# Kernel optimization log

Measured on AMD Instinct MI355X. Metric: run time of the kernel, lower is better.

Reference implementation:

```python
import jax, jax.numpy as jnp
import numpy as np
import math

N = 20000          # nodes
E = 320000         # edges (avg degree 16)
NS, NV = 16, 4     # scalar / vector multiplicities
NCAT = 10
CAT_VOCAB = 119
DIST_DIM = 32
LIG_MAX_R = 5.0
W1_NUMEL = NS * NS + NS * NV          # 320 : layer1 tp weights
W2_NUMEL = NS * NS + NV * NS + NS * NV + NV * NV + NV * NV  # 416


def setup_inputs() -> dict:
    key = jax.random.key(0)
    ks = jax.random.split(key, 24)
    s = 0.1
    inp = {
        'x_cat': jax.random.randint(ks[0], (N, NCAT), 0, 2),
        'x_scalar': jax.random.normal(ks[1], (N, 32), jnp.float32),
        'pos': jax.random.normal(ks[2], (N, 3), jnp.float32) * 3.0,
        'edge_index': jax.random.randint(ks[3], (2, E), 0, N),
        'edge_bond': jax.random.uniform(ks[4], (E, 10), jnp.float32),
        # AtomEncoder params
        'emb_tables': jax.random.normal(ks[5], (NCAT, CAT_VOCAB, NS)) * s,
        'node_w': jax.random.normal(ks[6], (32, NS)) * s,
        'node_b': jnp.zeros((NS,), jnp.float32),
        # lig_edge_embedding MLP (42 -> ns -> ns)
        'em_w1': jax.random.normal(ks[7], (10 + DIST_DIM, NS)) * s,
        'em_b1': jnp.zeros((NS,), jnp.float32),
        'em_w2': jax.random.normal(ks[8], (NS, NS)) * s,
        'em_b2': jnp.zeros((NS,), jnp.float32),
        'c1_w1': jax.random.normal(ks[9], (3 * NS, 3 * NS)) * s,
        'c1_b1': jnp.zeros((3 * NS,), jnp.float32),
        'c1_w2': jax.random.normal(ks[10], (3 * NS, W1_NUMEL)) * s,
        'c1_b2': jnp.zeros((W1_NUMEL,), jnp.float32),
        # conv layer 2 fc
        'c2_w1': jax.random.normal(ks[11], (3 * NS, 3 * NS)) * s,
        'c2_b1': jnp.zeros((3 * NS,), jnp.float32),
        'c2_w2': jax.random.normal(ks[12], (3 * NS, W2_NUMEL)) * s,
        'c2_b2': jnp.zeros((W2_NUMEL,), jnp.float32),
    }
    return inp


def _scatter_mean(vals, idx, n):
    s = jax.ops.segment_sum(vals, idx, num_segments=n)
    cnt = jax.ops.segment_sum(jnp.ones(idx.shape, vals.dtype), idx, num_segments=n)
    return s / jnp.maximum(cnt, 1.0)[:, None]


def _forward(x_cat, x_scalar, pos, edge_index, edge_bond,
             emb_tables, node_w, node_b, em_w1, em_b1, em_w2, em_b2,
             c1_w1, c1_b1, c1_w2, c1_b2, c2_w1, c2_b1, c2_w2, c2_b2):
    ns, nv = NS, NV
    n = x_cat.shape[0]
    # ---- AtomEncoder: sum of categorical embeddings + linear(scalar) ----
    gathered = emb_tables[jnp.arange(NCAT)[None, :], x_cat]      # [N, 10, ns]
    node = gathered.sum(axis=1) + x_scalar @ node_w + node_b    # [N, ns]

    src, dst = edge_index[0], edge_index[1]
    vec = pos[dst] - pos[src]                                   # [E, 3]
    dist = jnp.sqrt(jnp.sum(vec * vec, axis=-1) + 1e-12)
    unit = vec / (dist + 1e-8)[:, None]
    # spherical harmonics, lmax=1, component normalization: [1, sqrt(3)*r_hat]
    sh0 = jnp.ones((vec.shape[0], 1), vec.dtype)
    sh1 = math.sqrt(3.0) * unit                                 # [E, 3]

    # ---- GaussianSmearing + edge embedding MLP ----
    offset = jnp.linspace(0.0, LIG_MAX_R, DIST_DIM)
    coeff = -0.5 / float(LIG_MAX_R / (DIST_DIM - 1)) ** 2
    demb = jnp.exp(coeff * (dist[:, None] - offset[None, :]) ** 2)
    e_in = jnp.concatenate([edge_bond, demb], axis=1)           # [E, 42]
    edge_emb = jax.nn.relu(e_in @ em_w1 + em_b1) @ em_w2 + em_b2  # [E, ns]

    # ======== conv layer 1: ns x0e -> ns x0e + nv x1o ========
    ea = jnp.concatenate([edge_emb, node[src, :ns], node[dst, :ns]], axis=1)
    w = jax.nn.relu(ea @ c1_w1 + c1_b1) @ c1_w2 + c1_b2         # [E, 320]
    wa = w[:, :ns * ns].reshape(-1, ns, ns)
    wb = w[:, ns * ns:].reshape(-1, ns, nv)
    s_dst = node[dst]                                           # [E, ns]
    a = 1.0 / math.sqrt(ns)                                     # fan-in norm
    out0 = jnp.einsum('euk,eu->ek', wa, s_dst) * sh0 * a        # 0e x 0e -> 0e
    out1 = jnp.einsum('euw,eu->ew', wb, s_dst)[:, :, None] * sh1[:, None, :] * a
    tp = jnp.concatenate([out0, out1.reshape(-1, 3 * nv)], axis=1)
    node = _scatter_mean(tp, src, n)                            # [N, ns+3nv]

    # ======== conv layer 2: ns x0e + nv x1o -> ns x0e + nv x1o + nv x1e ====
    ea = jnp.concatenate([edge_emb, node[src, :ns], node[dst, :ns]], axis=1)
    w = jax.nn.relu(ea @ c2_w1 + c2_b1) @ c2_w2 + c2_b2         # [E, 416]
    o = 0
    wa = w[:, o:o + ns * ns].reshape(-1, ns, ns); o += ns * ns
    wb = w[:, o:o + nv * ns].reshape(-1, nv, ns); o += nv * ns
    wc = w[:, o:o + ns * nv].reshape(-1, ns, nv); o += ns * nv
    wd = w[:, o:o + nv * nv].reshape(-1, nv, nv); o += nv * nv
    we = w[:, o:o + nv * nv].reshape(-1, nv, nv)
    s = node[dst, :ns]
    v = node[dst, ns:].reshape(-1, nv, 3)
    a0 = 1.0 / math.sqrt(ns + nv)   # two paths into 0e
    a1 = 1.0 / math.sqrt(ns + nv)   # two paths into 1o
    aE = 1.0 / math.sqrt(nv)        # one path into 1e
    vdot = jnp.einsum('evi,ei->ev', v, sh1)                     # 1o . 1o
    out0 = (jnp.einsum('euk,eu->ek', wa, s) * sh0
            + jnp.einsum('euk,eu->ek', wb, vdot) / math.sqrt(3.0)) * a0
    out1o = (jnp.einsum('euw,eu->ew', wc, s)[:, :, None] * sh1[:, None, :]
             + jnp.einsum('euw,eui->ewi', wd, v) * sh0[:, :, None]) * a1
    crossv = jnp.cross(v, jnp.broadcast_to(sh1[:, None, :], v.shape))
    out1e = jnp.einsum('euw,eui->ewi', we, crossv) * (aE / math.sqrt(2.0))
    tp = jnp.concatenate([out0, out1o.reshape(-1, 3 * nv),
                          out1e.reshape(-1, 3 * nv)], axis=1)
    node = _scatter_mean(tp, src, n)                            # [N, ns+6nv] = [N,40]
    return node


def reference(x_cat, x_scalar, pos, edge_index, edge_bond,
              emb_tables, node_w, node_b, em_w1, em_b1, em_w2, em_b2,
              c1_w1, c1_b1, c1_w2, c1_b2, c2_w1, c2_b1, c2_w2, c2_b2):
    return _forward(x_cat, x_scalar, pos, edge_index, edge_bond,
                    emb_tables, node_w, node_b, em_w1, em_b1, em_w2, em_b2,
                    c1_w1, c1_b1, c1_w2, c1_b2, c2_w1, c2_b1, c2_w2, c2_b2)
```

## Files before the change

kernel.cpp:

```cpp
#include <hip/hip_runtime.h>
#include <math.h>

#define NN 20000
#define NE 320000

typedef _Float16 f16x8 __attribute__((ext_vector_type(8)));
typedef float f32x4 __attribute__((ext_vector_type(4)));
typedef unsigned short ushort_t;
typedef unsigned int uint_t;

#define MFMA16(A,B,C) __builtin_amdgcn_mfma_f32_16x16x32_f16((A),(B),(C),0,0,0)
#define LDS_FENCE() do{ asm volatile("s_waitcnt lgkmcnt(0)" ::: "memory"); __builtin_amdgcn_sched_barrier(0);}while(0)

static_assert(NE % 64 == 0, "edge grid must tile exactly");

__device__ __forceinline__ float frelu(float x){ return fmaxf(x, 0.0f); }

__device__ __forceinline__ void splitf(float x, ushort_t& h, ushort_t& l){
    _Float16 hh = (_Float16)x;
    float r = (x - (float)hh) * 2048.0f;
    _Float16 ll = (_Float16)r;
    union { _Float16 f; ushort_t u; } ch, cl;
    ch.f = hh; cl.f = ll;
    h = ch.u; l = cl.u;
}

__device__ __forceinline__ void edge_embed(
    int e, int s, int d,
    const float* __restrict__ pos,
    const float* __restrict__ edge_bond,
    const float* __restrict__ em_w1, const float* __restrict__ em_b1,
    const float* __restrict__ em_w2, const float* __restrict__ em_b2,
    float* eemb, float* sh1)
{
    float vx = pos[d*3+0] - pos[s*3+0];
    float vy = pos[d*3+1] - pos[s*3+1];
    float vz = pos[d*3+2] - pos[s*3+2];
    float d2 = vx*vx + vy*vy + vz*vz + 1e-12f;
    float dist = sqrtf(d2);
    float inv = 1.0f / (dist + 1e-8f);
    const float SQ3 = 1.7320508075688772f;
    sh1[0] = SQ3 * vx * inv;
    sh1[1] = SQ3 * vy * inv;
    sh1[2] = SQ3 * vz * inv;

    float ein[42];
    #pragma unroll
    for (int t = 0; t < 10; ++t) ein[t] = edge_bond[e*10 + t];
    const float coeff = -19.22f;
    const float step  = 5.0f / 31.0f;
    #pragma unroll
    for (int k = 0; k < 32; ++k) {
        float dd = dist - step * (float)k;
        ein[10+k] = __expf(coeff * dd * dd);
    }

    float t1[16];
    #pragma unroll
    for (int j = 0; j < 16; ++j) t1[j] = em_b1[j];
    #pragma unroll
    for (int t = 0; t < 42; ++t) {
        float v = ein[t];
        #pragma unroll
        for (int j = 0; j < 16; ++j) t1[j] += v * em_w1[t*16 + j];
    }
    #pragma unroll
    for (int j = 0; j < 16; ++j) t1[j] = frelu(t1[j]);

    #pragma unroll
    for (int j = 0; j < 16; ++j) eemb[j] = em_b2[j];
    #pragma unroll
    for (int t = 0; t < 16; ++t) {
        float v = t1[t];
        #pragma unroll
        for (int j = 0; j < 16; ++j) eemb[j] += v * em_w2[t*16 + j];
    }
}

__global__ __launch_bounds__(256)
void k_node_y(const float* __restrict__ node, int stride,
              const float* __restrict__ w1, float* __restrict__ y)
{
    int n = blockIdx.x*256 + threadIdx.x;
    if (n >= NN) return;
    float sv[16];
    const float4* r = reinterpret_cast<const float4*>(node + (size_t)n*stride);
    #pragma unroll
    for (int k = 0; k < 4; ++k) {
        float4 q = r[k];
        sv[4*k]=q.x; sv[4*k+1]=q.y; sv[4*k+2]=q.z; sv[4*k+3]=q.w;
    }
    float yb[48];
    #pragma unroll
    for (int j = 0; j < 48; ++j) yb[j] = 0.f;
    #pragma unroll
    for (int t = 0; t < 16; ++t) {
        float v = sv[t];
        #pragma unroll
        for (int j = 0; j < 48; ++j) yb[j] += v * w1[(16+t)*48 + j];
    }
    float* yo = y + (size_t)n*96;
    #pragma unroll
    for (int j = 0; j < 12; ++j)
        reinterpret_cast<float4*>(yo)[j] = make_float4(yb[4*j], yb[4*j+1], yb[4*j+2], yb[4*j+3]);
    #pragma unroll
    for (int j = 0; j < 48; ++j) yb[j] = 0.f;
    #pragma unroll
    for (int t = 0; t < 16; ++t) {
        float v = sv[t];
        #pragma unroll
        for (int j = 0; j < 48; ++j) yb[j] += v * w1[(32+t)*48 + j];
    }
    #pragma unroll
    for (int j = 0; j < 12; ++j)
        reinterpret_cast<float4*>(yo + 48)[j] = make_float4(yb[4*j], yb[4*j+1], yb[4*j+2], yb[4*j+3]);
}

__global__ __launch_bounds__(256)
void k_pack(const float* __restrict__ w2, const float* __restrict__ b2,
            ushort_t* __restrict__ out, int NC, int ntiles)
{
    int slot = blockIdx.x*256 + threadIdx.x;
    if (slot >= ntiles*128) return;
    int tl = slot >> 7; int r7 = slot & 127; int kb = r7 >> 6; int ll = r7 & 63;
    int col = tl*16 + (ll & 15);
    int k0 = (kb<<5) + ((ll>>4)<<3);
    uint_t hw[4], lw[4];
    #pragma unroll
    for (int p = 0; p < 4; ++p) {
        int ka = k0 + 2*p, kb2 = k0 + 2*p + 1;
        float va = (ka < 48) ? w2[ka*NC + col] : (ka == 48 ? b2[col] : 0.0f);
        float vb = (kb2 < 48) ? w2[kb2*NC + col] : (kb2 == 48 ? b2[col] : 0.0f);
        ushort_t ah, al, bh, bl;
        splitf(va, ah, al);
        splitf(vb, bh, bl);
        hw[p] = (uint_t)ah | ((uint_t)bh << 16);
        lw[p] = (uint_t)al | ((uint_t)bl << 16);
    }
    int base = tl*2048 + kb*1024 + ll*8;
    *reinterpret_cast<uint4*>(&out[base])       = make_uint4(hw[0], hw[1], hw[2], hw[3]);
    *reinterpret_cast<uint4*>(&out[base + 512]) = make_uint4(lw[0], lw[1], lw[2], lw[3]);
}

struct B4 { f16x8 h0, l0, h1, l1; };
__device__ __forceinline__ B4 loadB(const f16x8* __restrict__ g, int t, int l) {
    B4 b;
    const f16x8* p = g + t*256 + l;
    b.h0 = p[0];
    b.l0 = p[64];
    b.h1 = p[128];
    b.l1 = p[192];
    return b;
}

__device__ __forceinline__ void stage_A(ushort_t* bounce, int l,
                                        const uint_t* hph, const uint_t* hpl,
                                        f16x8 ahi[4][2], f16x8 alo[4][2])
{
    #pragma unroll
    for (int t = 0; t < 4; ++t)
        *reinterpret_cast<uint4*>(&bounce[l*32 + t*8]) = make_uint4(0,0,0,0);
    LDS_FENCE();
    #pragma unroll
    for (int mt = 0; mt < 4; ++mt) {
        if ((l >> 4) == mt) {
            #pragma unroll
            for (int jj = 0; jj < 25; ++jj) {
                int k = jj*2, kb = k >> 5, kk = k & 31;
                int lr = (l & 15) + ((kk >> 3) << 4);
                int off = kb*512 + lr*8 + (kk & 7);
                *reinterpret_cast<uint_t*>(&bounce[off])        = hph[jj];
                *reinterpret_cast<uint_t*>(&bounce[1024 + off]) = hpl[jj];
            }
        }
        LDS_FENCE();
        ahi[mt][0] = *reinterpret_cast<const f16x8*>(&bounce[l*8]);
        ahi[mt][1] = *reinterpret_cast<const f16x8*>(&bounce[512 + l*8]);
        alo[mt][0] = *reinterpret_cast<const f16x8*>(&bounce[1024 + l*8]);
        alo[mt][1] = *reinterpret_cast<const f16x8*>(&bounce[1536 + l*8]);
        LDS_FENCE();
    }
}

__device__ __forceinline__ void build_h_reg(
    const float* em, int s, int d,
    const float* __restrict__ y,
    const float* __restrict__ w1, const float* __restrict__ b1,
    float* h)
{
    #pragma unroll
    for (int j = 0; j < 48; ++j) h[j] = b1[j];
    #pragma unroll
    for (int t = 0; t < 16; ++t) {
        float v = em[t];
        #pragma unroll
        for (int j = 0; j < 48; ++j) h[j] += v * w1[t*48 + j];
    }
    const float4* pb = reinterpret_cast<const float4*>(y + (size_t)s*96);
    const float4* pc = reinterpret_cast<const float4*>(y + (size_t)d*96 + 48);
    #pragma unroll
    for (int kk = 0; kk < 12; ++kk) {
        float4 qb = pb[kk], qc = pc[kk];
        h[4*kk+0] = frelu(h[4*kk+0] + qb.x + qc.x);
        h[4*kk+1] = frelu(h[4*kk+1] + qb.y + qc.y);
        h[4*kk+2] = frelu(h[4*kk+2] + qb.z + qc.z);
        h[4*kk+3] = frelu(h[4*kk+3] + qb.w + qc.w);
    }
}

__global__ __launch_bounds__(256)
void k_node_feat(const int* __restrict__ x_cat, const float* __restrict__ x_scalar,
                 const float* __restrict__ emb, const float* __restrict__ node_w,
                 const float* __restrict__ node_b, float* __restrict__ node0)
{
    int n = blockIdx.x * 256 + threadIdx.x;
    if (n >= NN) return;
    float acc[16];
    #pragma unroll
    for (int k = 0; k < 16; ++k) acc[k] = node_b[k];
    #pragma unroll
    for (int c = 0; c < 10; ++c) {
        int idx = x_cat[n*10 + c];
        const float4* row = reinterpret_cast<const float4*>(emb + (c*119 + idx)*16);
        #pragma unroll
        for (int k = 0; k < 4; ++k) {
            float4 q = row[k];
            acc[4*k+0] += q.x; acc[4*k+1] += q.y; acc[4*k+2] += q.z; acc[4*k+3] += q.w;
        }
    }
    #pragma unroll
    for (int t = 0; t < 32; ++t) {
        float xs = x_scalar[n*32 + t];
        #pragma unroll
        for (int k = 0; k < 16; ++k) acc[k] += xs * node_w[t*16 + k];
    }
    #pragma unroll
    for (int k = 0; k < 16; ++k) node0[n*16 + k] = acc[k];
}

__global__ __launch_bounds__(64)
void k_edge_l1(const int* __restrict__ ei, const float* __restrict__ pos,
               const float* __restrict__ edge_bond,
               const float* __restrict__ em_w1, const float* __restrict__ em_b1,
               const float* __restrict__ em_w2, const float* __restrict__ em_b2,
               const float* __restrict__ w1, const float* __restrict__ b1,
               const ushort_t* __restrict__ packW,
               const float* __restrict__ y,
               const float* __restrict__ node0,
               float* __restrict__ eembG, float* __restrict__ eshG,
               float* __restrict__ accum, float* __restrict__ cnt)
{
    __shared__ __align__(16) unsigned char smem[5376];
    float* sT  = (float*)smem;
    float* sSh = (float*)(smem + 4352);
    int*   sSrc= (int*)(smem + 5120);

    int l = threadIdx.x;
    int cc = l & 15;
    int e = blockIdx.x*64 + l;
    int s = ei[e], d = ei[NE + e];

    float em[16], sh1[3];
    edge_embed(e, s, d, pos, edge_bond, em_w1, em_b1, em_w2, em_b2, em, sh1);
    {
        float4* pe = reinterpret_cast<float4*>(eembG + (size_t)e*16);
        #pragma unroll
        for (int k = 0; k < 4; ++k)
            pe[k] = make_float4(em[4*k], em[4*k+1], em[4*k+2], em[4*k+3]);
        reinterpret_cast<float4*>(eshG)[e] = make_float4(sh1[0], sh1[1], sh1[2], 0.f);
    }
    atomicAdd(cnt + s, 1.0f);

    float sd[16];
    {
        const float4* rd = reinterpret_cast<const float4*>(node0 + (size_t)d*16);
        #pragma unroll
        for (int k = 0; k < 4; ++k) {
            float4 q = rd[k];
            sd[4*k]=q.x; sd[4*k+1]=q.y; sd[4*k+2]=q.z; sd[4*k+3]=q.w;
        }
    }
    float h[48];
    build_h_reg(em, s, d, y, w1, b1, h);

    uint_t hph[25], hpl[25];
    #pragma unroll
    for (int jj = 0; jj < 24; ++jj) {
        ushort_t ah, al, bh, bl;
        splitf(h[2*jj],   ah, al);
        splitf(h[2*jj+1], bh, bl);
        hph[jj] = (uint_t)ah | ((uint_t)bh << 16);
        hpl[jj] = (uint_t)al | ((uint_t)bl << 16);
    }
    hph[24] = 0x3C00u;
    hpl[24] = 0u;

    f16x8 ahi[4][2], alo[4][2];
    stage_A((ushort_t*)smem, l, hph, hpl, ahi, alo);

    LDS_FENCE();
    sSrc[l] = s;
    #pragma unroll
    for (int u = 0; u < 16; ++u) sT[u*68 + l] = sd[u];
    sSh[l*3+0] = sh1[0]; sSh[l*3+1] = sh1[1]; sSh[l*3+2] = sh1[2];
    LDS_FENCE();

    f32x4 out0[4];
    float ob[4][4];
    #pragma unroll
    for (int mt = 0; mt < 4; ++mt) {
        out0[mt] = (f32x4){0.f,0.f,0.f,0.f};
        #pragma unroll
        for (int r = 0; r < 4; ++r) ob[mt][r] = 0.f;
    }

    const f16x8* gB = reinterpret_cast<const f16x8*>(packW);

    auto process = [&](int t, const B4& cur) {
        #pragma unroll
        for (int mt = 0; mt < 4; ++mt) {
            f32x4 Dh = (f32x4){0.f,0.f,0.f,0.f};
            f32x4 Dc = (f32x4){0.f,0.f,0.f,0.f};
            Dh = MFMA16(ahi[mt][0], cur.h0, Dh);
            Dh = MFMA16(ahi[mt][1], cur.h1, Dh);
            Dc = MFMA16(alo[mt][0], cur.h0, Dc);
            Dc = MFMA16(ahi[mt][0], cur.l0, Dc);
            Dc = MFMA16(alo[mt][1], cur.h1, Dc);
            Dc = MFMA16(ahi[mt][1], cur.l1, Dc);
            f32x4 D = Dh + Dc * 0.00048828125f;
            int elb = (mt << 4) + ((l >> 4) << 2);
            if (t < 16) {
                f32x4 sv = *reinterpret_cast<const f32x4*>(&sT[t*68 + elb]);
                out0[mt] += sv * D;
            } else {
                const float* sp = &sT[(((t-16)<<2) + (cc>>2))*68 + elb];
                #pragma unroll
                for (int r = 0; r < 4; ++r) ob[mt][r] += sp[r] * D[r];
            }
        }
    };

    B4 b0 = loadB(gB, 0, l), b1v = loadB(gB, 1, l);
    #pragma unroll 1
    for (int t = 0; t < 20; t += 2) {
        B4 p0 = (t + 2 < 20) ? loadB(gB, t + 2, l) : b0;
        process(t, b0);
        B4 p1 = (t + 3 < 20) ? loadB(gB, t + 3, l) : b1v;
        process(t + 1, b1v);
        b0 = p0; b1v = p1;
    }

    #pragma unroll
    for (int mt = 0; mt < 4; ++mt) {
        int elb = (mt << 4) + ((l >> 4) << 2);
        #pragma unroll
        for (int r = 0; r < 4; ++r) {
            int el = elb + r;
            int sidx = sSrc[el];
            atomicAdd(accum + (size_t)sidx*28 + cc, out0[mt][r] * 0.25f);
            float x = ob[mt][r];
            x += __shfl_xor(x, 4); x += __shfl_xor(x, 8);
            int q = cc / 3; int i2 = cc - q*3;
            float xq = __shfl(x, (l & 48) | q);
            if (cc < 12)
                atomicAdd(accum + (size_t)sidx*28 + 16 + cc, 0.25f * xq * sSh[el*3 + i2]);
        }
    }
}

__global__ __launch_bounds__(64)
void k_edge_l2(const int* __restrict__ ei,
               const float* __restrict__ w1, const float* __restrict__ b1,
               const ushort_t* __restrict__ packW,
               const float* __restrict__ eembG, const float* __restrict__ eshG,
               const float* __restrict__ y,
               const float* __restrict__ node1,
               float* __restrict__ accum2)
{
    __shared__ __align__(16) unsigned char smem[9728];
    float* sT  = (float*)smem;
    float* sVd = (float*)(smem + 4352);
    float* sV  = (float*)(smem + 5440);
    float* sSh = (float*)(smem + 8704);
    int*   sSrc= (int*)(smem + 9472);

    int l = threadIdx.x;
    int cc = l & 15;
    int e = blockIdx.x*64 + l;
    int s = ei[e], d = ei[NE + e];

    float4 shv = reinterpret_cast<const float4*>(eshG)[e];
    float sh1[3] = {shv.x, shv.y, shv.z};
    float sd[16], vv[12];
    {
        const float4* rd = reinterpret_cast<const float4*>(node1 + (size_t)d*28);
        #pragma unroll
        for (int k = 0; k < 4; ++k) {
            float4 q = rd[k];
            sd[4*k]=q.x; sd[4*k+1]=q.y; sd[4*k+2]=q.z; sd[4*k+3]=q.w;
        }
        #pragma unroll
        for (int k = 0; k < 3; ++k) {
            float4 q = rd[4+k];
            vv[4*k]=q.x; vv[4*k+1]=q.y; vv[4*k+2]=q.z; vv[4*k+3]=q.w;
        }
    }
    float vdr[4];
    const float INV_SQ3 = 0.5773502691896258f;
    #pragma unroll
    for (int u = 0; u < 4; ++u)
        vdr[u] = (vv[u*3]*sh1[0] + vv[u*3+1]*sh1[1] + vv[u*3+2]*sh1[2]) * INV_SQ3;

    float em[16];
    {
        const float4* pe = reinterpret_cast<const float4*>(eembG + (size_t)e*16);
        #pragma unroll
        for (int k = 0; k < 4; ++k) {
            float4 q = pe[k];
            em[4*k]=q.x; em[4*k+1]=q.y; em[4*k+2]=q.z; em[4*k+3]=q.w;
        }
    }
    float h[48];
    build_h_reg(em, s, d, y, w1, b1, h);

    uint_t hph[25], hpl[25];
    #pragma unroll
    for (int jj = 0; jj < 24; ++jj) {
        ushort_t ah, al, bh, bl;
        splitf(h[2*jj],   ah, al);
        splitf(h[2*jj+1], bh, bl);
        hph[jj] = (uint_t)ah | ((uint_t)bh << 16);
        hpl[jj] = (uint_t)al | ((uint_t)bl << 16);
    }
    hph[24] = 0x3C00u;
    hpl[24] = 0u;

    f16x8 ahi[4][2], alo[4][2];
    stage_A((ushort_t*)smem, l, hph, hpl, ahi, alo);

    LDS_FENCE();
    sSrc[l] = s;
    #pragma unroll
    for (int u = 0; u < 16; ++u) sT[u*68 + l] = sd[u];
    #pragma unroll
    for (int u = 0; u < 4; ++u) sVd[u*68 + l] = vdr[u];
    #pragma unroll
    for (int k = 0; k < 12; ++k) sV[k*68 + l] = vv[k];
    sSh[l*3+0] = sh1[0]; sSh[l*3+1] = sh1[1]; sSh[l*3+2] = sh1[2];
    LDS_FENCE();

    const float A0 = 0.22360679774997896f;
    const float AE = 0.3535533905932738f;

    f32x4 out0[4];
    float outc[4][4];
    #pragma unroll
    for (int mt = 0; mt < 4; ++mt) {
        out0[mt] = (f32x4){0.f,0.f,0.f,0.f};
        #pragma unroll
        for (int r = 0; r < 4; ++r) outc[mt][r] = 0.f;
    }

    const f16x8* gB = reinterpret_cast<const f16x8*>(packW);

    auto process = [&](int t, const B4& cur) {
        #pragma unroll
        for (int mt = 0; mt < 4; ++mt) {
            f32x4 Dh = (f32x4){0.f,0.f,0.f,0.f};
            f32x4 Dc = (f32x4){0.f,0.f,0.f,0.f};
            Dh = MFMA16(ahi[mt][0], cur.h0, Dh);
            Dh = MFMA16(ahi[mt][1], cur.h1, Dh);
            Dc = MFMA16(alo[mt][0], cur.h0, Dc);
            Dc = MFMA16(ahi[mt][0], cur.l0, Dc);
            Dc = MFMA16(alo[mt][1], cur.h1, Dc);
            Dc = MFMA16(ahi[mt][1], cur.l1, Dc);
            f32x4 D = Dh + Dc * 0.00048828125f;
            int elb = (mt << 4) + ((l >> 4) << 2);
            if (t < 16) {
                f32x4 sv = *reinterpret_cast<const f32x4*>(&sT[t*68 + elb]);
                out0[mt] += sv * D;
            } else if (t < 20) {
                f32x4 vd = *reinterpret_cast<const f32x4*>(&sVd[(t-16)*68 + elb]);
                out0[mt] += vd * D;
            } else if (t < 24) {
                const float* sp = &sT[(((t-20)<<2) + (cc>>2))*68 + elb];
                #pragma unroll
                for (int r = 0; r < 4; ++r) outc[mt][r] += sp[r] * D[r];
            } else if (t == 24) {
                int base3 = (cc >> 2) * 3;
                #pragma unroll
                for (int r = 0; r < 4; ++r) {
                    int el = elb + r;
                    float vx = sV[(base3+0)*68 + el];
                    float vy = sV[(base3+1)*68 + el];
                    float vz = sV[(base3+2)*68 + el];
                    float a0 = D[r]*vx, a1 = D[r]*vy, a2 = D[r]*vz;
                    a0 += __shfl_xor(a0,4); a0 += __shfl_xor(a0,8);
                    a1 += __shfl_xor(a1,4); a1 += __shfl_xor(a1,8);
                    a2 += __shfl_xor(a2,4); a2 += __shfl_xor(a2,8);
                    float xc = outc[mt][r];
                    xc += __shfl_xor(xc,4); xc += __shfl_xor(xc,8);
                    int q = cc / 3; int i2 = cc - q*3;
                    int srcl = (l & 48) | q;
                    float g0 = __shfl(a0, srcl), g1 = __shfl(a1, srcl), g2 = __shfl(a2, srcl);
                    float oo = (i2==0) ? g0 : ((i2==1) ? g1 : g2);
                    float xq = __shfl(xc, srcl);
                    if (cc < 12) {
                        float sh1i = sSh[el*3 + i2];
                        atomicAdd(accum2 + (size_t)sSrc[el]*40 + 16 + cc,
                                  A0 * (xq * sh1i + oo));
                    }
                }
            } else {
                int base3 = (cc >> 2) * 3;
                #pragma unroll
                for (int r = 0; r < 4; ++r) {
                    int el = elb + r;
                    float vx = sV[(base3+0)*68 + el];
                    float vy = sV[(base3+1)*68 + el];
                    float vz = sV[(base3+2)*68 + el];
                    float sx = sSh[el*3+0], sy = sSh[el*3+1], sz = sSh[el*3+2];
                    float cx = vy*sz - vz*sy;
                    float cy = vz*sx - vx*sz;
                    float cz = vx*sy - vy*sx;
                    float a0 = D[r]*cx, a1 = D[r]*cy, a2 = D[r]*cz;
                    a0 += __shfl_xor(a0,4); a0 += __shfl_xor(a0,8);
                    a1 += __shfl_xor(a1,4); a1 += __shfl_xor(a1,8);
                    a2 += __shfl_xor(a2,4); a2 += __shfl_xor(a2,8);
                    int q = cc / 3; int i2 = cc - q*3;
                    int srcl = (l & 48) | q;
                    float g0 = __shfl(a0, srcl), g1 = __shfl(a1, srcl), g2 = __shfl(a2, srcl);
                    float oo = (i2==0) ? g0 : ((i2==1) ? g1 : g2);
                    if (cc < 12)
                        atomicAdd(accum2 + (size_t)sSrc[el]*40 + 28 + cc, AE * oo);
                }
            }
        }
    };

    B4 b0 = loadB(gB, 0, l), b1v = loadB(gB, 1, l);
    #pragma unroll 1
    for (int t = 0; t < 26; t += 2) {
        B4 p0 = (t + 2 < 26) ? loadB(gB, t + 2, l) : b0;
        process(t, b0);
        B4 p1 = (t + 3 < 26) ? loadB(gB, t + 3, l) : b1v;
        process(t + 1, b1v);
        b0 = p0; b1v = p1;
    }

    #pragma unroll
    for (int mt = 0; mt < 4; ++mt) {
        int elb = (mt << 4) + ((l >> 4) << 2);
        #pragma unroll
        for (int r = 0; r < 4; ++r) {
            int el = elb + r;
            atomicAdd(accum2 + (size_t)sSrc[el]*40 + cc, out0[mt][r] * A0);
        }
    }
}

__global__ __launch_bounds__(256)
void k_div(const float* __restrict__ in, float* __restrict__ out,
           const float* __restrict__ cnt, int cols, int total)
{
    int i = blockIdx.x * 256 + threadIdx.x;
    if (i >= total) return;
    int n = i / cols;
    out[i] = in[i] / fmaxf(cnt[n], 1.0f);
}

extern "C" void kernel_launch(void* const* d_in, const int* in_sizes, int n_in,
                              void* d_out, int out_size, void* d_ws, size_t ws_size,
                              hipStream_t stream) {
    const int*   x_cat     = (const int*)  d_in[0];
    const float* x_scalar  = (const float*)d_in[1];
    const float* pos       = (const float*)d_in[2];
    const int*   ei        = (const int*)  d_in[3];
    const float* edge_bond = (const float*)d_in[4];
    const float* emb       = (const float*)d_in[5];
    const float* node_w    = (const float*)d_in[6];
    const float* node_b    = (const float*)d_in[7];
    const float* em_w1     = (const float*)d_in[8];
    const float* em_b1     = (const float*)d_in[9];
    const float* em_w2     = (const float*)d_in[10];
    const float* em_b2     = (const float*)d_in[11];
    const float* c1_w1     = (const float*)d_in[12];
    const float* c1_b1     = (const float*)d_in[13];
    const float* c1_w2     = (const float*)d_in[14];
    const float* c1_b2     = (const float*)d_in[15];
    const float* c2_w1     = (const float*)d_in[16];
    const float* c2_b1     = (const float*)d_in[17];
    const float* c2_w2     = (const float*)d_in[18];
    const float* c2_b2     = (const float*)d_in[19];

    float* ws    = (float*)d_ws;
    float* node0 = ws;
    float* accum1= ws + 320000;
    float* accum2= ws + 880000;
    float* cnt   = ws + 1680000;
    float* node1 = ws + 1700000;
    ushort_t* packA = (ushort_t*)(ws + 2260000);
    ushort_t* packB = packA + 20*2048;
    float* eembG = ws + 2307104;
    float* eshG  = ws + 7427104;
    float* yBuf  = ws + 8707104;

    hipMemsetAsync(accum1, 0, (size_t)(560000 + 800000 + 20000) * sizeof(float), stream);

    k_pack<<<(20*128 + 255) / 256, 256, 0, stream>>>(c1_w2, c1_b2, packA, 320, 20);
    k_pack<<<(26*128 + 255) / 256, 256, 0, stream>>>(c2_w2, c2_b2, packB, 416, 26);

    k_node_feat<<<(NN + 255) / 256, 256, 0, stream>>>(
        x_cat, x_scalar, emb, node_w, node_b, node0);

    k_node_y<<<(NN + 255) / 256, 256, 0, stream>>>(node0, 16, c1_w1, yBuf);

    k_edge_l1<<<NE / 64, 64, 0, stream>>>(
        ei, pos, edge_bond, em_w1, em_b1, em_w2, em_b2,
        c1_w1, c1_b1, packA, yBuf, node0, eembG, eshG, accum1, cnt);

    k_div<<<(560000 + 255) / 256, 256, 0, stream>>>(accum1, node1, cnt, 28, 560000);

    k_node_y<<<(NN + 255) / 256, 256, 0, stream>>>(node1, 28, c2_w1, yBuf);

    k_edge_l2<<<NE / 64, 64, 0, stream>>>(
        ei, c2_w1, c2_b1, packB, eembG, eshG, yBuf, node1, accum2);

    k_div<<<(800000 + 255) / 256, 256, 0, stream>>>(accum2, (float*)d_out, cnt, 40, 800000);
}
```

Baseline: 330.8 us.

## Sort edges by source via CSR permutation and segment-reduce before atomics

Builds a counting-sort permutation of edges by source node (degree count, single-block scan, scatter) each call, and processes edges in that order in both edge kernels. Within each 64-edge wavefront, contiguous runs sharing a source are summed in LDS and flushed with one atomic per segment and column instead of one per edge, and node degree comes from the row pointers instead of a float atomic count. This cuts global atomic traffic but adds three small preprocessing kernels, including a serial single-block scan, and makes the per-edge gathers through perm less coalesced.

```diff
diff --git a/kernel.cpp b/kernel.cpp
--- a/kernel.cpp
+++ b/kernel.cpp
@@ -78,6 +78,47 @@
 }
 
 __global__ __launch_bounds__(256)
+void k_deg(const int* __restrict__ ei, int* __restrict__ deg)
+{
+    int e = blockIdx.x*256 + threadIdx.x;
+    if (e < NE) atomicAdd(&deg[ei[e]], 1);
+}
+
+__global__ __launch_bounds__(256)
+void k_scan(const int* __restrict__ deg, int* __restrict__ rowptr, int* __restrict__ off)
+{
+    __shared__ int part[256];
+    int t = threadIdx.x;
+    const int chunk = (NN + 255) / 256;
+    int lo = t*chunk, hi = lo + chunk; if (hi > NN) hi = NN; if (lo > NN) lo = NN;
+    int s = 0;
+    for (int i = lo; i < hi; ++i) s += deg[i];
+    part[t] = s;
+    __syncthreads();
+    for (int ofs = 1; ofs < 256; ofs <<= 1) {
+        int v = (t >= ofs) ? part[t-ofs] : 0;
+        __syncthreads();
+        part[t] += v;
+        __syncthreads();
+    }
+    int run = (t == 0) ? 0 : part[t-1];
+    for (int i = lo; i < hi; ++i) {
+        rowptr[i] = run; off[i] = run;
+        run += deg[i];
+    }
+    if (t == 255) rowptr[NN] = NE;
+}
+
+__global__ __launch_bounds__(256)
+void k_scatter(const int* __restrict__ ei, int* __restrict__ off, int* __restrict__ perm)
+{
+    int e = blockIdx.x*256 + threadIdx.x;
+    if (e >= NE) return;
+    int p = atomicAdd(&off[ei[e]], 1);
+    perm[p] = e;
+}
+
+__global__ __launch_bounds__(256)
 void k_node_y(const float* __restrict__ node, int stride,
               const float* __restrict__ w1, float* __restrict__ y)
 {
@@ -182,6 +223,24 @@
     }
 }
 
+__device__ __forceinline__ void seg_reduce(const float* sTP, const int* sSrc,
+                                           unsigned long long heads, int l,
+                                           int ncols, int c0, int C,
+                                           float* __restrict__ accum)
+{
+    while (heads) {
+        int start = __ffsll((unsigned long long)heads) - 1;
+        unsigned long long rest = heads & (heads - 1);
+        int end = rest ? (__ffsll((unsigned long long)rest) - 1) : 64;
+        if (l < ncols) {
+            float sum = 0.f;
+            for (int r = start; r < end; ++r) sum += sTP[r*16 + l];
+            atomicAdd(accum + (size_t)sSrc[start]*C + c0 + l, sum);
+        }
+        heads = rest;
+    }
+}
+
 __device__ __forceinline__ void build_h_reg(
     const float* em, int s, int d,
     const float* __restrict__ y,
@@ -247,8 +306,9 @@
                const ushort_t* __restrict__ packW,
                const float* __restrict__ y,
                const float* __restrict__ node0,
+               const int* __restrict__ perm,
                float* __restrict__ eembG, float* __restrict__ eshG,
-               float* __restrict__ accum, float* __restrict__ cnt)
+               float* __restrict__ accum)
 {
     __shared__ __align__(16) unsigned char smem[5376];
     float* sT  = (float*)smem;
@@ -257,19 +317,22 @@
 
     int l = threadIdx.x;
     int cc = l & 15;
-    int e = blockIdx.x*64 + l;
+    int i = blockIdx.x*64 + l;
+    int e = perm[i];
     int s = ei[e], d = ei[NE + e];
+
+    int sprev = __shfl_up(s, 1);
+    unsigned long long heads = __ballot((l == 0) || (s != sprev));
 
     float em[16], sh1[3];
     edge_embed(e, s, d, pos, edge_bond, em_w1, em_b1, em_w2, em_b2, em, sh1);
     {
-        float4* pe = reinterpret_cast<float4*>(eembG + (size_t)e*16);
+        float4* pe = reinterpret_cast<float4*>(eembG + (size_t)i*16);
         #pragma unroll
         for (int k = 0; k < 4; ++k)
             pe[k] = make_float4(em[4*k], em[4*k+1], em[4*k+2], em[4*k+3]);
-        reinterpret_cast<float4*>(eshG)[e] = make_float4(sh1[0], sh1[1], sh1[2], 0.f);
-    }
-    atomicAdd(cnt + s, 1.0f);
+        reinterpret_cast<float4*>(eshG)[i] = make_float4(sh1[0], sh1[1], sh1[2], 0.f);
+    }
 
     float sd[16];
     {
@@ -350,22 +413,35 @@
         b0 = p0; b1v = p1;
     }
 
+    float* sTP = sT;
+    LDS_FENCE();
     #pragma unroll
     for (int mt = 0; mt < 4; ++mt) {
         int elb = (mt << 4) + ((l >> 4) << 2);
         #pragma unroll
+        for (int r = 0; r < 4; ++r)
+            sTP[(elb + r)*16 + cc] = out0[mt][r] * 0.25f;
+    }
+    LDS_FENCE();
+    seg_reduce(sTP, sSrc, heads, l, 16, 0, 28, accum);
+    LDS_FENCE();
+
+    #pragma unroll
+    for (int mt = 0; mt < 4; ++mt) {
+        int elb = (mt << 4) + ((l >> 4) << 2);
+        #pragma unroll
         for (int r = 0; r < 4; ++r) {
             int el = elb + r;
-            int sidx = sSrc[el];
-            atomicAdd(accum + (size_t)sidx*28 + cc, out0[mt][r] * 0.25f);
             float x = ob[mt][r];
             x += __shfl_xor(x, 4); x += __shfl_xor(x, 8);
             int q = cc / 3; int i2 = cc - q*3;
             float xq = __shfl(x, (l & 48) | q);
             if (cc < 12)
-                atomicAdd(accum + (size_t)sidx*28 + 16 + cc, 0.25f * xq * sSh[el*3 + i2]);
-        }
-    }
+                sTP[el*16 + cc] = 0.25f * xq * sSh[el*3 + i2];
+        }
+    }
+    LDS_FENCE();
+    seg_reduce(sTP, sSrc, heads, l, 12, 16, 28, accum);
 }
 
 __global__ __launch_bounds__(64)
@@ -375,6 +451,7 @@
                const float* __restrict__ eembG, const float* __restrict__ eshG,
                const float* __restrict__ y,
                const float* __restrict__ node1,
+               const int* __restrict__ perm,
                float* __restrict__ accum2)
 {
     __shared__ __align__(16) unsigned char smem[9728];
@@ -386,10 +463,14 @@
 
     int l = threadIdx.x;
     int cc = l & 15;
-    int e = blockIdx.x*64 + l;
+    int i = blockIdx.x*64 + l;
+    int e = perm[i];
     int s = ei[e], d = ei[NE + e];
 
-    float4 shv = reinterpret_cast<const float4*>(eshG)[e];
+    int sprev = __shfl_up(s, 1);
+    unsigned long long heads = __ballot((l == 0) || (s != sprev));
+
+    float4 shv = reinterpret_cast<const float4*>(eshG)[i];
     float sh1[3] = {shv.x, shv.y, shv.z};
     float sd[16], vv[12];
     {
@@ -413,7 +494,7 @@
 
     float em[16];
     {
-        const float4* pe = reinterpret_cast<const float4*>(eembG + (size_t)e*16);
+        const float4* pe = reinterpret_cast<const float4*>(eembG + (size_t)i*16);
         #pragma unroll
         for (int k = 0; k < 4; ++k) {
             float4 q = pe[k];
@@ -462,6 +543,7 @@
     }
 
     const f16x8* gB = reinterpret_cast<const f16x8*>(packW);
+    float* sTP = sT;
 
     auto process = [&](int t, const B4& cur) {
         #pragma unroll
@@ -507,8 +589,7 @@
                     float xq = __shfl(xc, srcl);
                     if (cc < 12) {
                         float sh1i = sSh[el*3 + i2];
-                        atomicAdd(accum2 + (size_t)sSrc[el]*40 + 16 + cc,
-                                  A0 * (xq * sh1i + oo));
+                        sTP[el*16 + cc] = A0 * (xq * sh1i + oo);
                     }
                 }
             } else {
@@ -532,7 +613,7 @@
                     float g0 = __shfl(a0, srcl), g1 = __shfl(a1, srcl), g2 = __shfl(a2, srcl);
                     float oo = (i2==0) ? g0 : ((i2==1) ? g1 : g2);
                     if (cc < 12)
-                        atomicAdd(accum2 + (size_t)sSrc[el]*40 + 28 + cc, AE * oo);
+                        sTP[el*16 + cc] = AE * oo;
                 }
             }
         }
@@ -540,33 +621,41 @@
 
     B4 b0 = loadB(gB, 0, l), b1v = loadB(gB, 1, l);
     #pragma unroll 1
-    for (int t = 0; t < 26; t += 2) {
-        B4 p0 = (t + 2 < 26) ? loadB(gB, t + 2, l) : b0;
+    for (int t = 0; t < 24; t += 2) {
+        B4 p0 = loadB(gB, t + 2, l);
         process(t, b0);
-        B4 p1 = (t + 3 < 26) ? loadB(gB, t + 3, l) : b1v;
+        B4 p1 = loadB(gB, t + 3, l);
         process(t + 1, b1v);
         b0 = p0; b1v = p1;
     }
-
+    process(24, b0);
+    LDS_FENCE();
+    seg_reduce(sTP, sSrc, heads, l, 12, 16, 40, accum2);
+    LDS_FENCE();
+    process(25, b1v);
+    LDS_FENCE();
+    seg_reduce(sTP, sSrc, heads, l, 12, 28, 40, accum2);
+    LDS_FENCE();
     #pragma unroll
     for (int mt = 0; mt < 4; ++mt) {
         int elb = (mt << 4) + ((l >> 4) << 2);
         #pragma unroll
-        for (int r = 0; r < 4; ++r) {
-            int el = elb + r;
-            atomicAdd(accum2 + (size_t)sSrc[el]*40 + cc, out0[mt][r] * A0);
-        }
-    }
+        for (int r = 0; r < 4; ++r)
+            sTP[(elb + r)*16 + cc] = out0[mt][r] * A0;
+    }
+    LDS_FENCE();
+    seg_reduce(sTP, sSrc, heads, l, 16, 0, 40, accum2);
 }
 
 __global__ __launch_bounds__(256)
 void k_div(const float* __restrict__ in, float* __restrict__ out,
-           const float* __restrict__ cnt, int cols, int total)
+           const int* __restrict__ rowp, int cols, int total)
 {
     int i = blockIdx.x * 256 + threadIdx.x;
     if (i >= total) return;
     int n = i / cols;
-    out[i] = in[i] / fmaxf(cnt[n], 1.0f);
+    float c = (float)(rowp[n+1] - rowp[n]);
+    out[i] = in[i] / fmaxf(c, 1.0f);
 }
 
 extern "C" void kernel_launch(void* const* d_in, const int* in_sizes, int n_in,
@@ -597,15 +686,23 @@
     float* node0 = ws;
     float* accum1= ws + 320000;
     float* accum2= ws + 880000;
-    float* cnt   = ws + 1680000;
-    float* node1 = ws + 1700000;
-    ushort_t* packA = (ushort_t*)(ws + 2260000);
+    float* node1 = ws + 1680000;
+    int*   degI  = (int*)(ws + 2240000);
+    int*   rowp  = (int*)(ws + 2260000);
+    int*   offI  = (int*)(ws + 2280008);
+    int*   permI = (int*)(ws + 2300008);
+    ushort_t* packA = (ushort_t*)(ws + 2620008);
     ushort_t* packB = packA + 20*2048;
-    float* eembG = ws + 2307104;
-    float* eshG  = ws + 7427104;
-    float* yBuf  = ws + 8707104;
-
-    hipMemsetAsync(accum1, 0, (size_t)(560000 + 800000 + 20000) * sizeof(float), stream);
+    float* eembG = ws + 2667112;
+    float* eshG  = ws + 7787112;
+    float* yBuf  = ws + 9067112;
+
+    hipMemsetAsync(degI, 0, 20000 * sizeof(int), stream);
+    hipMemsetAsync(accum1, 0, (size_t)(560000 + 800000) * sizeof(float), stream);
+
+    k_deg<<<(NE + 255) / 256, 256, 0, stream>>>(ei, degI);
+    k_scan<<<1, 256, 0, stream>>>(degI, rowp, offI);
+    k_scatter<<<(NE + 255) / 256, 256, 0, stream>>>(ei, offI, permI);
 
     k_pack<<<(20*128 + 255) / 256, 256, 0, stream>>>(c1_w2, c1_b2, packA, 320, 20);
     k_pack<<<(26*128 + 255) / 256, 256, 0, stream>>>(c2_w2, c2_b2, packB, 416, 26);
@@ -617,14 +714,14 @@
 
     k_edge_l1<<<NE / 64, 64, 0, stream>>>(
         ei, pos, edge_bond, em_w1, em_b1, em_w2, em_b2,
-        c1_w1, c1_b1, packA, yBuf, node0, eembG, eshG, accum1, cnt);
-
-    k_div<<<(560000 + 255) / 256, 256, 0, stream>>>(accum1, node1, cnt, 28, 560000);
+        c1_w1, c1_b1, packA, yBuf, node0, permI, eembG, eshG, accum1);
+
+    k_div<<<(560000 + 255) / 256, 256, 0, stream>>>(accum1, node1, rowp, 28, 560000);
 
     k_node_y<<<(NN + 255) / 256, 256, 0, stream>>>(node1, 28, c2_w1, yBuf);
 
     k_edge_l2<<<NE / 64, 64, 0, stream>>>(
-        ei, c2_w1, c2_b1, packB, eembG, eshG, yBuf, node1, accum2);
-
-    k_div<<<(800000 + 255) / 256, 256, 0, stream>>>(accum2, (float*)d_out, cnt, 40, 800000);
-}
+        ei, c2_w1, c2_b1, packB, eembG, eshG, yBuf, node1, permI, accum2);
+
+    k_div<<<(800000 + 255) / 256, 256, 0, stream>>>(accum2, (float*)d_out, rowp, 40, 800000);
+}
```

New measurement: 391.2 us. +18.3%, slower.
